# Optimization experiments

Measured on AMD Instinct MI355X. Metric: run time of the kernel, lower is better.

The kernel has to match this reference:

```python
import jax, jax.numpy as jnp
import numpy as np

N = 100000
E = 1600000
F_IN = 256
HID = 8
HEADS = 8
CLS = 40
NEG_SLOPE = 0.2


def gat_conv(x, src, dst, W, a_src, a_dst, b, heads, ch, concat, num_nodes):
    # linear transform -> [N, H, C]
    h = (x @ W).reshape(num_nodes, heads, ch)
    # per-node attention logits [N, H]
    alpha_src = jnp.sum(h * a_src[None], axis=-1)
    alpha_dst = jnp.sum(h * a_dst[None], axis=-1)
    # per-edge logits gathered from endpoints [E, H]
    e = jax.nn.leaky_relu(alpha_src[src] + alpha_dst[dst], NEG_SLOPE)
    # segment softmax over edges grouped by destination node
    e_max = jax.ops.segment_max(e, dst, num_segments=num_nodes)
    ex = jnp.exp(e - e_max[dst])
    denom = jax.ops.segment_sum(ex, dst, num_segments=num_nodes)
    alpha = ex / denom[dst]  # every node has a self-loop, so denom > 0
    # weighted scatter-aggregate of source features [N, H, C]
    out = jax.ops.segment_sum(h[src] * alpha[..., None], dst, num_segments=num_nodes)
    if concat:
        out = out.reshape(num_nodes, heads * ch)
    else:
        out = out.mean(axis=1)
    return out + b


def setup_inputs() -> dict:
    key = jax.random.key(0)
    ks = jax.random.split(key, 10)
    x = jax.random.normal(ks[0], (N, F_IN), dtype=jnp.float32)
    edge_index = jax.random.randint(ks[1], (2, E), 0, N, dtype=jnp.int64)
    s1 = 1.0 / np.sqrt(F_IN)
    s2 = 1.0 / np.sqrt(HID * HEADS)
    W1 = jax.random.normal(ks[2], (F_IN, HEADS * HID), dtype=jnp.float32) * s1
    a_src1 = jax.random.normal(ks[3], (HEADS, HID), dtype=jnp.float32) * s1
    a_dst1 = jax.random.normal(ks[4], (HEADS, HID), dtype=jnp.float32) * s1
    b1 = jnp.zeros((HEADS * HID,), dtype=jnp.float32)
    W2 = jax.random.normal(ks[5], (HEADS * HID, CLS), dtype=jnp.float32) * s2
    a_src2 = jax.random.normal(ks[6], (1, CLS), dtype=jnp.float32) * s2
    a_dst2 = jax.random.normal(ks[7], (1, CLS), dtype=jnp.float32) * s2
    b2 = jnp.zeros((CLS,), dtype=jnp.float32)
    return {"x": x, "edge_index": edge_index, "W1": W1, "a_src1": a_src1,
            "a_dst1": a_dst1, "b1": b1, "W2": W2, "a_src2": a_src2,
            "a_dst2": a_dst2, "b2": b2}


def reference(x, edge_index, W1, a_src1, a_dst1, b1, W2, a_src2, a_dst2, b2):
    # PyG GATConv adds self-loops by default
    loops = jnp.arange(N, dtype=edge_index.dtype)
    src = jnp.concatenate([edge_index[0], loops])
    dst = jnp.concatenate([edge_index[1], loops])
    # eval mode: dropout is identity
    h = gat_conv(x, src, dst, W1, a_src1, a_dst1, b1, HEADS, HID, True, N)
    h = jax.nn.elu(h)
    out = gat_conv(h, src, dst, W2, a_src2, a_dst2, b2, 1, CLS, False, N)
    return jax.nn.log_softmax(out, axis=1)
```

## Files before the change

### kernel.cpp

```cpp
#include <hip/hip_runtime.h>
#include <hip/hip_bf16.h>

#define NN 100000
#define NE 1600000
#define ETOT (NE + NN)
#define FIN 256
#define CLS 40
#define NSLOPE 0.2f

#define BKT_SHIFT 8
#define BKT_NODES 256
#define NB ((NN + BKT_NODES - 1) / BKT_NODES)
#define CAP 8192
#define EPB 4096
#define NBLK_BIN ((ETOT + EPB - 1) / EPB)
#define NGRP (NN / 16)
#define NBLK_AGG2 ((NGRP + 3) / 4)

typedef __attribute__((ext_vector_type(8))) __bf16 bf16x8;
typedef __attribute__((ext_vector_type(8))) unsigned short us8;
typedef __attribute__((ext_vector_type(4))) float f32x4;

__device__ __forceinline__ unsigned short f2b(float f) {
  union { float f; unsigned int u; } c; c.f = f;
  unsigned int u = c.u + 0x7fffu + ((c.u >> 16) & 1u);
  return (unsigned short)(u >> 16);
}
__device__ __forceinline__ float b2f(unsigned short u) {
  union { unsigned int u; float f; } c; c.u = (unsigned int)u << 16;
  return c.f;
}

__device__ __forceinline__ int load_idx(const void* ei, long long pos, int is64) {
  if (is64) return (int)((const long long*)ei)[pos];
  return ((const int*)ei)[pos];
}

__global__ void detect_kernel(const int* ei32, int* flag, int* bcur) {
  for (int i = threadIdx.x; i < NB; i += 64) bcur[i] = i * CAP;
  if (threadIdx.x == 0) {
    int is64 = 1;
    for (int i = 0; i < 64; ++i) if (ei32[2 * i + 1] != 0) { is64 = 0; break; }
    *flag = is64;
  }
}

__global__ __launch_bounds__(256) void bin_scatter_kernel(const void* __restrict__ ei,
                                                          const int* __restrict__ flag,
                                                          int* __restrict__ bcur,
                                                          unsigned int* __restrict__ binned) {
  __shared__ int lcnt[NB];
  __shared__ int lbase[NB];
  for (int i = threadIdx.x; i < NB; i += 256) lcnt[i] = 0;
  __syncthreads();
  const int is64 = *flag;
  const long long e0 = (long long)blockIdx.x * EPB;
  int rank[EPB / 256];
  int bb[EPB / 256];
  unsigned int pk[EPB / 256];
  #pragma unroll
  for (int k = 0; k < EPB / 256; ++k) {
    long long e = e0 + k * 256 + threadIdx.x;
    rank[k] = -1;
    if (e < ETOT) {
      int src, dst;
      if (e < NE) { src = load_idx(ei, e, is64); dst = load_idx(ei, (long long)NE + e, is64); }
      else        { src = dst = (int)(e - NE); }
      int b = dst >> BKT_SHIFT;
      bb[k] = b;
      pk[k] = ((unsigned int)(dst & 255) << 24) | (unsigned int)src;
      rank[k] = atomicAdd(&lcnt[b], 1);
    }
  }
  __syncthreads();
  for (int i = threadIdx.x; i < NB; i += 256)
    lbase[i] = lcnt[i] ? atomicAdd(&bcur[i], lcnt[i]) : 0;
  __syncthreads();
  #pragma unroll
  for (int k = 0; k < EPB / 256; ++k)
    if (rank[k] >= 0) binned[(size_t)lbase[bb[k]] + rank[k]] = pk[k];
}

__global__ __launch_bounds__(256) void csr_kernel(const unsigned int* __restrict__ binned,
                                                  const int* __restrict__ bcur,
                                                  int* __restrict__ offs,
                                                  int* __restrict__ deg,
                                                  int* __restrict__ esrc,
                                                  unsigned char* __restrict__ eloc) {
  __shared__ int ncnt[BKT_NODES];
  __shared__ int ncur[BKT_NODES];
  __shared__ int wsum[4];
  const int b = blockIdx.x;
  const int t = threadIdx.x;
  const int node0 = b << BKT_SHIFT;
  const int ebeg = b * CAP, eend = bcur[b];
  ncnt[t] = 0;
  __syncthreads();
  for (int i = ebeg + t; i < eend; i += 256) {
    int dstl = (int)(binned[i] >> 24);
    atomicAdd(&ncnt[dstl], 1);
  }
  __syncthreads();
  const int v = ncnt[t];
  const int lane = t & 63, w = t >> 6;
  int sc = v;
  #pragma unroll
  for (int off = 1; off < 64; off <<= 1) {
    int u = __shfl_up(sc, off);
    if (lane >= off) sc += u;
  }
  if (lane == 63) wsum[w] = sc;
  __syncthreads();
  int woff = 0;
  for (int i = 0; i < w; ++i) woff += wsum[i];
  const int gpos = ebeg + woff + sc - v;
  const int node = node0 + t;
  if (node < NN) { offs[node] = gpos; deg[node] = v; }
  ncur[t] = gpos;
  __syncthreads();
  for (int i = ebeg + t; i < eend; i += 256) {
    unsigned int p = binned[i];
    int dstl = (int)(p >> 24);
    int pos = atomicAdd(&ncur[dstl], 1);
    esrc[pos] = (int)(p & 0xffffffu);
    eloc[pos] = (unsigned char)dstl;
  }
}

#define BM 64
#define APAD 72
#define WP 72
__global__ __launch_bounds__(256) void gemm1_mfma_kernel(
    const float* __restrict__ x, const float* __restrict__ W1,
    unsigned short* __restrict__ h1b) {
  __shared__ unsigned short Wt[64 * WP];
  __shared__ unsigned short At[BM * APAD];
  const int tid = threadIdx.x;
  const int lane = tid & 63;
  const int wid = tid >> 6;
  const int m_base = blockIdx.x * BM;
  const int lrow = lane & 15;
  const int kgrp = lane >> 4;
  const int sub = tid & 15;
  const int rr  = tid >> 4;

  const float* xrow[4];
  #pragma unroll
  for (int i = 0; i < 4; ++i) {
    int row = m_base + i * 16 + rr;
    if (row >= NN) row = NN - 1;
    xrow[i] = x + (size_t)row * FIN + sub * 4;
  }

  float4 pfx[4], pfw[4];
  #pragma unroll
  for (int i = 0; i < 4; ++i) pfx[i] = *(const float4*)(xrow[i]);
  #pragma unroll
  for (int j = 0; j < 4; ++j)
    pfw[j] = *(const float4*)(W1 + (size_t)(j * 16 + rr) * 64 + sub * 4);

  f32x4 acc[4] = {};

  for (int ks = 0; ks < 4; ++ks) {
    __syncthreads();
    #pragma unroll
    for (int i = 0; i < 4; ++i) {
      ushort4 t4;
      t4.x = f2b(pfx[i].x); t4.y = f2b(pfx[i].y); t4.z = f2b(pfx[i].z); t4.w = f2b(pfx[i].w);
      *(ushort4*)(&At[(i * 16 + rr) * APAD + sub * 4]) = t4;
    }
    #pragma unroll
    for (int j = 0; j < 4; ++j) {
      const int kl = j * 16 + rr, n0 = sub * 4;
      Wt[(n0 + 0) * WP + kl] = f2b(pfw[j].x);
      Wt[(n0 + 1) * WP + kl] = f2b(pfw[j].y);
      Wt[(n0 + 2) * WP + kl] = f2b(pfw[j].z);
      Wt[(n0 + 3) * WP + kl] = f2b(pfw[j].w);
    }
    if (ks < 3) {
      #pragma unroll
      for (int i = 0; i < 4; ++i) pfx[i] = *(const float4*)(xrow[i] + (ks + 1) * 64);
      #pragma unroll
      for (int j = 0; j < 4; ++j)
        pfw[j] = *(const float4*)(W1 + (size_t)((ks + 1) * 64 + j * 16 + rr) * 64 + sub * 4);
    }
    __syncthreads();
    #pragma unroll
    for (int kk = 0; kk < 2; ++kk) {
      const int klocal = kk * 32 + kgrp * 8;
      const bf16x8 afrag = *(const bf16x8*)(&At[(wid * 16 + lrow) * APAD + klocal]);
      #pragma unroll
      for (int nt = 0; nt < 4; ++nt) {
        const bf16x8 bfrag = *(const bf16x8*)(&Wt[(nt * 16 + lrow) * WP + klocal]);
        acc[nt] = __builtin_amdgcn_mfma_f32_16x16x32_bf16(afrag, bfrag, acc[nt], 0, 0, 0);
      }
    }
  }

  #pragma unroll
  for (int reg = 0; reg < 4; ++reg) {
    const int row = m_base + wid * 16 + kgrp * 4 + reg;
    if (row < NN) {
      #pragma unroll
      for (int nt = 0; nt < 4; ++nt)
        h1b[(size_t)row * 64 + nt * 16 + lrow] = f2b(acc[nt][reg]);
    }
  }
}

__global__ __launch_bounds__(256) void alpha1_kernel(
    const unsigned short* __restrict__ h1b, const float* __restrict__ a_src,
    const float* __restrict__ a_dst,
    unsigned short* __restrict__ as1b, float* __restrict__ ad1) {
  const int g = blockIdx.x * 256 + threadIdx.x;
  const int node = g >> 3, head = g & 7;
  if (node >= NN) return;
  const us8 hv = *(const us8*)(h1b + (size_t)node * 64 + head * 8);
  float s = 0.f, d = 0.f;
  #pragma unroll
  for (int c = 0; c < 8; ++c) {
    float v = b2f(hv[c]);
    s += v * a_src[head * 8 + c];
    d += v * a_dst[head * 8 + c];
  }
  as1b[g] = f2b(s); ad1[g] = d;
}

__global__ __launch_bounds__(256) void agg1_kernel(
    const unsigned short* __restrict__ h1b, const unsigned short* __restrict__ as1b,
    const float* __restrict__ ad1, const float* __restrict__ b1,
    const int* __restrict__ offs, const int* __restrict__ deg,
    const int* __restrict__ esrc, float* __restrict__ out1) {
  __shared__ float exl[4][8][68];
  const int lane = threadIdx.x & 63;
  const int wid = threadIdx.x >> 6;
  const int n = __builtin_amdgcn_readfirstlane((int)(blockIdx.x * 4 + wid));
  const int beg = offs[n], end = beg + deg[n];
  const int hA = lane >> 3;
  const float4 ad0 = *(const float4*)(ad1 + n * 8);
  const float4 ad4 = *(const float4*)(ad1 + n * 8 + 4);
  const float adh[8] = {ad0.x, ad0.y, ad0.z, ad0.w, ad4.x, ad4.y, ad4.z, ad4.w};
  float dsum = 0.f, acc0 = 0.f, acc1 = 0.f;
  for (int base = beg; base < end; base += 64) {
    const int rem = end - base;
    int se = 0;
    float ex[8];
    if (lane < rem) {
      se = esrc[base + lane];
      const us8 a8 = *(const us8*)(as1b + (size_t)se * 8);
      #pragma unroll
      for (int h = 0; h < 8; ++h) {
        float t = b2f(a8[h]) + adh[h];
        t = t > 0.f ? t : NSLOPE * t;
        ex[h] = __expf(t);
      }
    } else {
      #pragma unroll
      for (int h = 0; h < 8; ++h) ex[h] = 0.f;
    }
    #pragma unroll
    for (int h = 0; h < 8; ++h) exl[wid][h][lane] = ex[h];
    const int nacc = rem < 64 ? rem : 64;
    for (int eg = 0; eg < 4; ++eg) {
      if (eg * 16 >= nacc) break;
      const float4 x0 = *(const float4*)(&exl[wid][hA][eg * 16]);
      const float4 x1 = *(const float4*)(&exl[wid][hA][eg * 16 + 4]);
      const float4 x2 = *(const float4*)(&exl[wid][hA][eg * 16 + 8]);
      const float4 x3 = *(const float4*)(&exl[wid][hA][eg * 16 + 12]);
      const float e16[16] = {x0.x, x0.y, x0.z, x0.w, x1.x, x1.y, x1.z, x1.w,
                             x2.x, x2.y, x2.z, x2.w, x3.x, x3.y, x3.z, x3.w};
      int seu[16];
      #pragma unroll
      for (int j = 0; j < 16; ++j) seu[j] = __builtin_amdgcn_readlane(se, eg * 16 + j);
      unsigned short r[16];
      #pragma unroll
      for (int j = 0; j < 16; ++j) r[j] = h1b[(size_t)seu[j] * 64 + lane];
      #pragma unroll
      for (int j = 0; j < 16; ++j) {
        dsum += e16[j];
        if (j & 1) acc1 += e16[j] * b2f(r[j]);
        else       acc0 += e16[j] * b2f(r[j]);
      }
    }
  }
  float val = (acc0 + acc1) / dsum + b1[lane];
  val = val > 0.f ? val : (__expf(val) - 1.f);
  out1[(size_t)n * 64 + lane] = val;
}

__global__ __launch_bounds__(256) void gemm2_kernel(
    const float* __restrict__ out1, const float* __restrict__ W2,
    const float* __restrict__ a_src2, const float* __restrict__ a_dst2,
    unsigned short* __restrict__ h2a, unsigned short* __restrict__ h2s,
    float* __restrict__ as2, float* __restrict__ ad2) {
  __shared__ float Wl[64 * CLS];
  __shared__ float asl[CLS], adl[CLS];
  for (int i = threadIdx.x; i < 64 * CLS; i += 256) Wl[i] = W2[i];
  if (threadIdx.x < CLS) { asl[threadIdx.x] = a_src2[threadIdx.x]; adl[threadIdx.x] = a_dst2[threadIdx.x]; }
  __syncthreads();
  const int lane = threadIdx.x & 63;
  const int wid = threadIdx.x >> 6;
  const int row0 = __builtin_amdgcn_readfirstlane((int)(blockIdx.x * 4 + wid) * 4);
  const float* xr = out1 + (size_t)row0 * 64;
  const int j = (lane < CLS) ? lane : 0;
  float acc[4] = {0.f, 0.f, 0.f, 0.f};
  #pragma unroll 8
  for (int k = 0; k < 64; ++k) {
    float w = Wl[k * CLS + j];
    acc[0] += xr[k]       * w;
    acc[1] += xr[k + 64]  * w;
    acc[2] += xr[k + 128] * w;
    acc[3] += xr[k + 192] * w;
  }
  #pragma unroll
  for (int r = 0; r < 4; ++r) {
    int row = row0 + r;
    float v = acc[r];
    float sa = (lane < CLS) ? v * asl[j] : 0.f;
    float sd = (lane < CLS) ? v * adl[j] : 0.f;
    for (int msk = 1; msk < 64; msk <<= 1) { sa += __shfl_xor(sa, msk); sd += __shfl_xor(sd, msk); }
    if (lane == 0) { as2[row] = sa; ad2[row] = sd; }
    if (lane < 32) h2a[(size_t)row * 32 + lane] = f2b(v);
    else if (lane < CLS) h2s[(size_t)row * 8 + lane - 32] = f2b(v);
  }
}

__global__ __launch_bounds__(256) void agg2_mfma_kernel(
    const unsigned short* __restrict__ h2a, const unsigned short* __restrict__ h2s,
    const float* __restrict__ as2, const float* __restrict__ ad2, const float* __restrict__ b2,
    const int* __restrict__ offs, const int* __restrict__ deg,
    const int* __restrict__ esrc, const unsigned char* __restrict__ eloc,
    float* __restrict__ out) {
  __shared__ unsigned short Alds[4][16][64];
  __shared__ int            sell[4][64];
  __shared__ float          ad2l[4][16];
  __shared__ float          dsumb[4][16];
  const int lane = threadIdx.x & 63;
  const int wid = threadIdx.x >> 6;
  const int g = blockIdx.x * 4 + wid;
  if (g >= NGRP) return;
  const int n0 = g * 16;
  const int kbeg = offs[n0];
  const int kend = offs[n0 + 15] + deg[n0 + 15];
  const int col = lane & 15;
  const int kg = lane >> 4;
  const int basek = kg * 8;
  if (lane < 16) ad2l[wid][lane] = ad2[n0 + lane];
  const float b2v0 = b2[col];
  const float b2v1 = b2[16 + col];
  const float b2v2 = (col < 8) ? b2[32 + col] : 0.f;
  us8 onesw;
  #pragma unroll
  for (int j = 0; j < 8; ++j) onesw[j] = (col == 0) ? (unsigned short)0x3F80 : (unsigned short)0;
  const bf16x8 b3frag = *(const bf16x8*)&onesw;

  f32x4 acc0 = {}, acc1 = {}, acc2 = {}, acc3 = {};
  const char* h2aC = (const char*)h2a;
  const char* h2sC = (const char*)h2s;

  for (int kb = kbeg; kb < kend; kb += 64) {
    const int rem = kend - kb;
    {
      f32x4 z = {};
      f32x4* Az = (f32x4*)&Alds[wid][0][0];
      Az[lane] = z;
      Az[lane + 64] = z;
    }
    int se = 0, loc = 0;
    if (lane < rem) {
      se = esrc[kb + lane];
      loc = (int)(eloc[kb + lane] & 15);
    }
    float t = as2[se] + ad2l[wid][loc];
    t = t > 0.f ? t : NSLOPE * t;
    const float ex = __expf(t);
    if (lane < rem) Alds[wid][loc][lane] = f2b(ex);
    sell[wid][lane] = (lane < rem) ? se : 0;
    #pragma unroll
    for (int s = 0; s < 2; ++s) {
      if (s * 32 >= rem) break;
      const bf16x8 afrag = *(const bf16x8*)&Alds[wid][col][s * 32 + basek];
      int sj[8];
      #pragma unroll
      for (int j = 0; j < 8; ++j) sj[j] = sell[wid][s * 32 + basek + j];
      us8 b0w, b1w, b2w;
      #pragma unroll
      for (int j = 0; j < 8; ++j) {
        const unsigned short* pA = (const unsigned short*)(h2aC + ((unsigned)sj[j] << 6)) + col;
        b0w[j] = pA[0];
        b1w[j] = pA[16];
        b2w[j] = *((const unsigned short*)(h2sC + ((unsigned)sj[j] << 4)) + col);
      }
      acc0 = __builtin_amdgcn_mfma_f32_16x16x32_bf16(afrag, *(const bf16x8*)&b0w, acc0, 0, 0, 0);
      acc1 = __builtin_amdgcn_mfma_f32_16x16x32_bf16(afrag, *(const bf16x8*)&b1w, acc1, 0, 0, 0);
      acc2 = __builtin_amdgcn_mfma_f32_16x16x32_bf16(afrag, *(const bf16x8*)&b2w, acc2, 0, 0, 0);
      acc3 = __builtin_amdgcn_mfma_f32_16x16x32_bf16(afrag, b3frag, acc3, 0, 0, 0);
    }
  }

  if (col == 0) *(f32x4*)&dsumb[wid][kg * 4] = acc3;
  const f32x4 dsv = *(const f32x4*)&dsumb[wid][kg * 4];

  #pragma unroll
  for (int reg = 0; reg < 4; ++reg) {
    const float inv = 1.f / dsv[reg];
    float v0 = acc0[reg] * inv + b2v0;
    float v1 = acc1[reg] * inv + b2v1;
    float v2 = acc2[reg] * inv + b2v2;
    float mx = fmaxf(v0, v1);
    if (col < 8) mx = fmaxf(mx, v2);
    #pragma unroll
    for (int msk = 1; msk < 16; msk <<= 1) mx = fmaxf(mx, __shfl_xor(mx, msk));
    float ss = __expf(v0 - mx) + __expf(v1 - mx) + ((col < 8) ? __expf(v2 - mx) : 0.f);
    #pragma unroll
    for (int msk = 1; msk < 16; msk <<= 1) ss += __shfl_xor(ss, msk);
    const float ls = __logf(ss) + mx;
    const int node = n0 + kg * 4 + reg;
    float* o = out + (size_t)node * CLS;
    o[col] = v0 - ls;
    o[16 + col] = v1 - ls;
    if (col < 8) o[32 + col] = v2 - ls;
  }
}

extern "C" void kernel_launch(void* const* d_in, const int* in_sizes, int n_in,
                              void* d_out, int out_size, void* d_ws, size_t ws_size,
                              hipStream_t stream) {
  (void)in_sizes; (void)n_in; (void)out_size; (void)ws_size;
  const float* x    = (const float*)d_in[0];
  const void*  ei   = d_in[1];
  const float* W1   = (const float*)d_in[2];
  const float* a_s1 = (const float*)d_in[3];
  const float* a_d1 = (const float*)d_in[4];
  const float* b1   = (const float*)d_in[5];
  const float* W2   = (const float*)d_in[6];
  const float* a_s2 = (const float*)d_in[7];
  const float* a_d2 = (const float*)d_in[8];
  const float* b2   = (const float*)d_in[9];
  float* out = (float*)d_out;

  char* ws = (char*)d_ws;
  size_t o = 256;
  int*   flag = (int*)(ws + 0);
  unsigned short* h1b = (unsigned short*)(ws + o); o += (size_t)NN * 64 * 2;
  unsigned short* as1b = (unsigned short*)(ws + o); o += (size_t)NN * 8 * 2 + 256;
  float* ad1  = (float*)(ws + o); o += (size_t)NN * 8 * 4;
  float* out1 = (float*)(ws + o); o += (size_t)NN * 64 * 4;
  unsigned short* h2a = (unsigned short*)(ws + o); o += (size_t)NN * 32 * 2;
  unsigned short* h2s = (unsigned short*)(ws + o); o += (size_t)NN * 8 * 2 + 256;
  float* as2  = (float*)(ws + o); o += (size_t)NN * 4;
  float* ad2  = (float*)(ws + o); o += (size_t)NN * 4;
  int*   offs = (int*)(ws + o);   o += (size_t)NN * 4 + 256;
  int*   deg  = (int*)(ws + o);   o += (size_t)NN * 4;
  int*   esrc = (int*)(ws + o);   o += (size_t)NB * CAP * 4;
  unsigned char* eloc = (unsigned char*)(ws + o); o += (size_t)NB * CAP + 256;
  int*   bcur = (int*)(ws + o);   o += (NB + 1) * 4;
  unsigned int* binned = (unsigned int*)out1;

  detect_kernel<<<1, 64, 0, stream>>>((const int*)ei, flag, bcur);
  gemm1_mfma_kernel<<<(NN + BM - 1) / BM, 256, 0, stream>>>(x, W1, h1b);
  bin_scatter_kernel<<<NBLK_BIN, 256, 0, stream>>>(ei, flag, bcur, binned);
  csr_kernel<<<NB, 256, 0, stream>>>(binned, bcur, offs, deg, esrc, eloc);
  alpha1_kernel<<<(NN * 8 + 255) / 256, 256, 0, stream>>>(h1b, a_s1, a_d1, as1b, ad1);
  agg1_kernel<<<NN / 4, 256, 0, stream>>>(h1b, as1b, ad1, b1, offs, deg, esrc, out1);
  gemm2_kernel<<<NN / 16, 256, 0, stream>>>(out1, W2, a_s2, a_d2, h2a, h2s, as2, ad2);
  agg2_mfma_kernel<<<NBLK_AGG2, 256, 0, stream>>>(h2a, h2s, as2, ad2, b2, offs, deg, esrc, eloc, out);
}
```

Before: 200.8 us.

## Fuse alpha1 into gemm1 epilogue, pack dst-local into esrc, interleave h2a

The per-node attention logit computation moves into the gemm1 epilogue, which stages the bf16 outputs in shared memory. This drops the alpha1 launch and its re-read of h1b. The separate eloc byte array is dropped: the packed (dst_local<<24|src) word is stored directly in esrc and unpacked in both aggregation kernels, saving one store stream and one load stream. h2a columns are interleaved so agg2 can fetch each pair of bf16 values with a single 32-bit gather instead of two 16-bit loads.

```diff
diff --git a/kernel.cpp b/kernel.cpp
--- a/kernel.cpp
+++ b/kernel.cpp
@@ -85,8 +85,7 @@
                                                   const int* __restrict__ bcur,
                                                   int* __restrict__ offs,
                                                   int* __restrict__ deg,
-                                                  int* __restrict__ esrc,
-                                                  unsigned char* __restrict__ eloc) {
+                                                  unsigned int* __restrict__ esrc) {
   __shared__ int ncnt[BKT_NODES];
   __shared__ int ncur[BKT_NODES];
   __shared__ int wsum[4];
@@ -122,8 +121,7 @@
     unsigned int p = binned[i];
     int dstl = (int)(p >> 24);
     int pos = atomicAdd(&ncur[dstl], 1);
-    esrc[pos] = (int)(p & 0xffffffu);
-    eloc[pos] = (unsigned char)dstl;
+    esrc[pos] = p;
   }
 }
 
@@ -132,7 +130,9 @@
 #define WP 72
 __global__ __launch_bounds__(256) void gemm1_mfma_kernel(
     const float* __restrict__ x, const float* __restrict__ W1,
-    unsigned short* __restrict__ h1b) {
+    const float* __restrict__ a_src, const float* __restrict__ a_dst,
+    unsigned short* __restrict__ h1b, unsigned short* __restrict__ as1b,
+    float* __restrict__ ad1) {
   __shared__ unsigned short Wt[64 * WP];
   __shared__ unsigned short At[BM * APAD];
   const int tid = threadIdx.x;
@@ -197,40 +197,40 @@
     }
   }
 
+  __syncthreads();
   #pragma unroll
   for (int reg = 0; reg < 4; ++reg) {
-    const int row = m_base + wid * 16 + kgrp * 4 + reg;
-    if (row < NN) {
-      #pragma unroll
-      for (int nt = 0; nt < 4; ++nt)
-        h1b[(size_t)row * 64 + nt * 16 + lrow] = f2b(acc[nt][reg]);
-    }
-  }
-}
-
-__global__ __launch_bounds__(256) void alpha1_kernel(
-    const unsigned short* __restrict__ h1b, const float* __restrict__ a_src,
-    const float* __restrict__ a_dst,
-    unsigned short* __restrict__ as1b, float* __restrict__ ad1) {
-  const int g = blockIdx.x * 256 + threadIdx.x;
-  const int node = g >> 3, head = g & 7;
-  if (node >= NN) return;
-  const us8 hv = *(const us8*)(h1b + (size_t)node * 64 + head * 8);
-  float s = 0.f, d = 0.f;
-  #pragma unroll
-  for (int c = 0; c < 8; ++c) {
-    float v = b2f(hv[c]);
-    s += v * a_src[head * 8 + c];
-    d += v * a_dst[head * 8 + c];
-  }
-  as1b[g] = f2b(s); ad1[g] = d;
+    const int lr = wid * 16 + kgrp * 4 + reg;
+    const int row = m_base + lr;
+    #pragma unroll
+    for (int nt = 0; nt < 4; ++nt) {
+      const unsigned short hb = f2b(acc[nt][reg]);
+      At[lr * APAD + nt * 16 + lrow] = hb;
+      if (row < NN) h1b[(size_t)row * 64 + nt * 16 + lrow] = hb;
+    }
+  }
+  __syncthreads();
+  #pragma unroll
+  for (int it = tid; it < 512; it += 256) {
+    const int lr = it >> 3, h = it & 7;
+    const int row = m_base + lr;
+    const us8 hv = *(const us8*)(&At[lr * APAD + h * 8]);
+    float s = 0.f, d = 0.f;
+    #pragma unroll
+    for (int c = 0; c < 8; ++c) {
+      const float v = b2f(hv[c]);
+      s += v * a_src[h * 8 + c];
+      d += v * a_dst[h * 8 + c];
+    }
+    if (row < NN) { as1b[row * 8 + h] = f2b(s); ad1[row * 8 + h] = d; }
+  }
 }
 
 __global__ __launch_bounds__(256) void agg1_kernel(
     const unsigned short* __restrict__ h1b, const unsigned short* __restrict__ as1b,
     const float* __restrict__ ad1, const float* __restrict__ b1,
     const int* __restrict__ offs, const int* __restrict__ deg,
-    const int* __restrict__ esrc, float* __restrict__ out1) {
+    const unsigned int* __restrict__ esrc, float* __restrict__ out1) {
   __shared__ float exl[4][8][68];
   const int lane = threadIdx.x & 63;
   const int wid = threadIdx.x >> 6;
@@ -246,7 +246,7 @@
     int se = 0;
     float ex[8];
     if (lane < rem) {
-      se = esrc[base + lane];
+      se = (int)(esrc[base + lane] & 0xffffffu);
       const us8 a8 = *(const us8*)(as1b + (size_t)se * 8);
       #pragma unroll
       for (int h = 0; h < 8; ++h) {
@@ -320,7 +320,7 @@
     float sd = (lane < CLS) ? v * adl[j] : 0.f;
     for (int msk = 1; msk < 64; msk <<= 1) { sa += __shfl_xor(sa, msk); sd += __shfl_xor(sd, msk); }
     if (lane == 0) { as2[row] = sa; ad2[row] = sd; }
-    if (lane < 32) h2a[(size_t)row * 32 + lane] = f2b(v);
+    if (lane < 32) h2a[(size_t)row * 32 + (lane & 15) * 2 + (lane >> 4)] = f2b(v);
     else if (lane < CLS) h2s[(size_t)row * 8 + lane - 32] = f2b(v);
   }
 }
@@ -329,8 +329,7 @@
     const unsigned short* __restrict__ h2a, const unsigned short* __restrict__ h2s,
     const float* __restrict__ as2, const float* __restrict__ ad2, const float* __restrict__ b2,
     const int* __restrict__ offs, const int* __restrict__ deg,
-    const int* __restrict__ esrc, const unsigned char* __restrict__ eloc,
-    float* __restrict__ out) {
+    const unsigned int* __restrict__ esrc, float* __restrict__ out) {
   __shared__ unsigned short Alds[4][16][64];
   __shared__ int            sell[4][64];
   __shared__ float          ad2l[4][16];
@@ -368,8 +367,9 @@
     }
     int se = 0, loc = 0;
     if (lane < rem) {
-      se = esrc[kb + lane];
-      loc = (int)(eloc[kb + lane] & 15);
+      const unsigned int p = esrc[kb + lane];
+      se = (int)(p & 0xffffffu);
+      loc = (int)(p >> 24) & 15;
     }
     float t = as2[se] + ad2l[wid][loc];
     t = t > 0.f ? t : NSLOPE * t;
@@ -386,9 +386,9 @@
       us8 b0w, b1w, b2w;
       #pragma unroll
       for (int j = 0; j < 8; ++j) {
-        const unsigned short* pA = (const unsigned short*)(h2aC + ((unsigned)sj[j] << 6)) + col;
-        b0w[j] = pA[0];
-        b1w[j] = pA[16];
+        const unsigned int pair = *(const unsigned int*)(h2aC + ((unsigned)sj[j] << 6) + col * 4);
+        b0w[j] = (unsigned short)(pair & 0xffffu);
+        b1w[j] = (unsigned short)(pair >> 16);
         b2w[j] = *((const unsigned short*)(h2sC + ((unsigned)sj[j] << 4)) + col);
       }
       acc0 = __builtin_amdgcn_mfma_f32_16x16x32_bf16(afrag, *(const bf16x8*)&b0w, acc0, 0, 0, 0);
@@ -452,17 +452,15 @@
   float* ad2  = (float*)(ws + o); o += (size_t)NN * 4;
   int*   offs = (int*)(ws + o);   o += (size_t)NN * 4 + 256;
   int*   deg  = (int*)(ws + o);   o += (size_t)NN * 4;
-  int*   esrc = (int*)(ws + o);   o += (size_t)NB * CAP * 4;
-  unsigned char* eloc = (unsigned char*)(ws + o); o += (size_t)NB * CAP + 256;
+  unsigned int* esrc = (unsigned int*)(ws + o); o += (size_t)NB * CAP * 4;
   int*   bcur = (int*)(ws + o);   o += (NB + 1) * 4;
   unsigned int* binned = (unsigned int*)out1;
 
   detect_kernel<<<1, 64, 0, stream>>>((const int*)ei, flag, bcur);
-  gemm1_mfma_kernel<<<(NN + BM - 1) / BM, 256, 0, stream>>>(x, W1, h1b);
+  gemm1_mfma_kernel<<<(NN + BM - 1) / BM, 256, 0, stream>>>(x, W1, a_s1, a_d1, h1b, as1b, ad1);
   bin_scatter_kernel<<<NBLK_BIN, 256, 0, stream>>>(ei, flag, bcur, binned);
-  csr_kernel<<<NB, 256, 0, stream>>>(binned, bcur, offs, deg, esrc, eloc);
-  alpha1_kernel<<<(NN * 8 + 255) / 256, 256, 0, stream>>>(h1b, a_s1, a_d1, as1b, ad1);
+  csr_kernel<<<NB, 256, 0, stream>>>(binned, bcur, offs, deg, esrc);
   agg1_kernel<<<NN / 4, 256, 0, stream>>>(h1b, as1b, ad1, b1, offs, deg, esrc, out1);
   gemm2_kernel<<<NN / 16, 256, 0, stream>>>(out1, W2, a_s2, a_d2, h2a, h2s, as2, ad2);
-  agg2_mfma_kernel<<<NBLK_AGG2, 256, 0, stream>>>(h2a, h2s, as2, ad2, b2, offs, deg, esrc, eloc, out);
-}
+  agg2_mfma_kernel<<<NBLK_AGG2, 256, 0, stream>>>(h2a, h2s, as2, ad2, b2, offs, deg, esrc, out);
+}
```

Measured after the change: 193.3 us. 1.04x faster.
